# Kernel tuning notes

Hardware: AMD Instinct MI355X
Metric: run time of the kernel (lower is better)

Reference implementation:

```python
import jax, jax.numpy as jnp
import numpy as np

EPS_BN = 1e-5


def _batchnorm(h, g, b):
    # training-mode BatchNorm1d over the flattened (B*N*k) axis
    mu = jnp.mean(h, axis=0)
    var = jnp.var(h, axis=0)
    return g * (h - mu) * jax.lax.rsqrt(var + EPS_BN) + b


def setup_inputs() -> dict:
    key = jax.random.key(0)
    ks = jax.random.split(key, 5)
    B, N = 4, 8192
    x = jax.random.normal(ks[0], (B, N, 3), dtype=jnp.float32)
    W1 = jax.random.normal(ks[1], (7, 10), dtype=jnp.float32) * (1.0 / np.sqrt(7.0))
    b1 = jax.random.normal(ks[2], (10,), dtype=jnp.float32) * 0.01
    W2 = jax.random.normal(ks[3], (10, 10), dtype=jnp.float32) * (1.0 / np.sqrt(10.0))
    b2 = jax.random.normal(ks[4], (10,), dtype=jnp.float32) * 0.01
    g1 = jnp.ones((10,), jnp.float32); be1 = jnp.zeros((10,), jnp.float32)
    g2 = jnp.ones((10,), jnp.float32); be2 = jnp.zeros((10,), jnp.float32)
    return {"x": x, "W1": W1, "b1": b1, "g1": g1, "be1": be1,
            "W2": W2, "b2": b2, "g2": g2, "be2": be2, "k": 9}


def reference(x, W1, b1, g1, be1, W2, b2, g2, be2, k):
    B, N, C = x.shape
    # --- kNN graph (brute force, self included as nearest) ---
    sq = jnp.sum(x * x, axis=-1)                                    # (B,N)
    d2 = sq[:, :, None] + sq[:, None, :] - 2.0 * jnp.einsum('bnc,bmc->bnm', x, x)
    _, idx = jax.lax.top_k(-d2, k + 1)                              # (B,N,k+1)
    nbrs = x[jnp.arange(B)[:, None, None], idx]                     # (B,N,k+1,3)
    rel = (nbrs - x[:, :, None, :])[:, :, 1:, :]                    # drop self -> (B,N,k,3)
    # --- sort neighbors by azimuth phi = atan2(y, x) ---
    phi = jnp.arctan2(rel[..., 1], rel[..., 0])                     # (B,N,k)
    order = jnp.argsort(phi, axis=-1)
    v1 = jnp.take_along_axis(rel, order[..., None], axis=2)         # (B,N,k,3)
    v2 = jnp.roll(v1, -1, axis=2)                                   # next neighbor (cyclic)
    # --- umbrella-style surface features ---
    centroids = 0.5 * (v1 + v2)
    normals = jnp.cross(v1, v2)
    normals = normals / (jnp.linalg.norm(normals, axis=-1, keepdims=True) + 1e-6)
    sign = jnp.where(normals[..., 0:1, 0] > 0, 1.0, -1.0)[..., None]  # (B,N,1,1)
    normals = normals * sign
    position = jnp.sum(normals * centroids, axis=-1, keepdims=True) / jnp.sqrt(jnp.asarray(3.0, x.dtype))
    feat = jnp.concatenate([centroids, normals, position], axis=-1)   # (B,N,k,7)
    feat = feat.reshape(B * N * k, 7)
    # --- tiny MLP + max-pool over k ---
    h = jax.nn.relu(_batchnorm(feat @ W1 + b1, g1, be1))
    h = jax.nn.relu(_batchnorm(h @ W2 + b2, g2, be2))
    return jnp.max(h.reshape(B, N, k, 10), axis=2)                  # (B,N,10)
```

## Files before the change

### kernel.cpp

```cpp
#include <hip/hip_runtime.h>
#include <math.h>
#include <float.h>
#include <stdint.h>

#define B_ 4
#define N_ 8192
#define K_ 9
#define NPTS (B_ * N_)
#define NROWS (NPTS * K_)
#define SPLIT 8
#define CHUNK (N_ / SPLIT)
#define NGROUP 32
#define GSIZE (CHUNK / NGROUP)
#define GSTRIDE 33

__device__ __forceinline__ float dist2f(float4 q, float4 c) {
  float dot = q.x * c.x + q.y * c.y + q.z * c.z;
  return (q.w + c.w) - 2.0f * dot;
}

#define GDECL(G) float gd##G; int gi##G;
#define SCANG(G)                                                           \
  { float bgd = FLT_MAX; int bgi = 0;                                      \
    _Pragma("clang loop unroll(disable)")                                  \
    for (int jj = 0; jj < GSIZE; jj += 4) {                                \
      const float4* cp = CH + (G * GSTRIDE + jj);                          \
      float4 c0 = cp[0], c1 = cp[1], c2 = cp[2], c3 = cp[3];               \
      int j = G * GSIZE + jj;                                              \
      float d0 = dist2f(q, c0), d1 = dist2f(q, c1);                        \
      float d2 = dist2f(q, c2), d3 = dist2f(q, c3);                        \
      if (HS) {                                                            \
        d0 = (j + 0 == nl) ? FLT_MAX : d0;                                 \
        d1 = (j + 1 == nl) ? FLT_MAX : d1;                                 \
        d2 = (j + 2 == nl) ? FLT_MAX : d2;                                 \
        d3 = (j + 3 == nl) ? FLT_MAX : d3;                                 \
      }                                                                    \
      bool l0 = d0 < bgd; bgd = l0 ? d0 : bgd; bgi = l0 ? (j + 0) : bgi;   \
      bool l1 = d1 < bgd; bgd = l1 ? d1 : bgd; bgi = l1 ? (j + 1) : bgi;   \
      bool l2 = d2 < bgd; bgd = l2 ? d2 : bgd; bgi = l2 ? (j + 2) : bgi;   \
      bool l3 = d3 < bgd; bgd = l3 ? d3 : bgd; bgi = l3 ? (j + 3) : bgi;   \
    }                                                                      \
    gd##G = bgd; gi##G = bgi; }
#define LM(G)                                                              \
  { bool lt = gd##G < wd;                                                  \
    wd = lt ? gd##G : wd; wi = lt ? gi##G : wi; wg = lt ? G : wg; }
#define WBK(G)                                                             \
  { bool m = (wg == G); gd##G = m ? nd : gd##G; gi##G = m ? ni : gi##G; }

template <bool HS>
__device__ __forceinline__ void knn_chunk(const float4* CH, float4 q, int nl,
                                          int j0, int s, int p,
                                          uint2* __restrict__ PBDI) {
  GDECL(0) GDECL(1) GDECL(2) GDECL(3) GDECL(4) GDECL(5) GDECL(6) GDECL(7)
  GDECL(8) GDECL(9) GDECL(10) GDECL(11) GDECL(12) GDECL(13) GDECL(14) GDECL(15)
  GDECL(16) GDECL(17) GDECL(18) GDECL(19) GDECL(20) GDECL(21) GDECL(22) GDECL(23)
  GDECL(24) GDECL(25) GDECL(26) GDECL(27) GDECL(28) GDECL(29) GDECL(30) GDECL(31)

  SCANG(0) SCANG(1) SCANG(2) SCANG(3) SCANG(4) SCANG(5) SCANG(6) SCANG(7)
  SCANG(8) SCANG(9) SCANG(10) SCANG(11) SCANG(12) SCANG(13) SCANG(14) SCANG(15)
  SCANG(16) SCANG(17) SCANG(18) SCANG(19) SCANG(20) SCANG(21) SCANG(22) SCANG(23)
  SCANG(24) SCANG(25) SCANG(26) SCANG(27) SCANG(28) SCANG(29) SCANG(30) SCANG(31)

#pragma clang loop unroll(disable)
  for (int r = 0; r < K_; ++r) {
    float wd = gd0; int wi = gi0; int wg = 0;
    LM(1) LM(2) LM(3) LM(4) LM(5) LM(6) LM(7)
    LM(8) LM(9) LM(10) LM(11) LM(12) LM(13) LM(14) LM(15)
    LM(16) LM(17) LM(18) LM(19) LM(20) LM(21) LM(22) LM(23)
    LM(24) LM(25) LM(26) LM(27) LM(28) LM(29) LM(30) LM(31)
    uint2 o; o.x = __float_as_uint(wd); o.y = (unsigned)(j0 + wi);
    PBDI[(size_t)(s * K_ + r) * NPTS + p] = o;

    int ab = wg * GSTRIDE;
    int jb = wg * GSIZE;
    float nd = FLT_MAX; int ni = 0;
#pragma clang loop unroll(disable)
    for (int jj = 0; jj < GSIZE; jj += 4) {
      const float4* cp = CH + (ab + jj);
      float4 c0 = cp[0], c1 = cp[1], c2 = cp[2], c3 = cp[3];
      int j = jb + jj;
      float d0 = dist2f(q, c0), d1 = dist2f(q, c1);
      float d2 = dist2f(q, c2), d3 = dist2f(q, c3);
      if (HS) {
        d0 = (j + 0 == nl) ? FLT_MAX : d0;
        d1 = (j + 1 == nl) ? FLT_MAX : d1;
        d2 = (j + 2 == nl) ? FLT_MAX : d2;
        d3 = (j + 3 == nl) ? FLT_MAX : d3;
      }
      bool k0 = (d0 > wd) | ((d0 == wd) & ((j + 0) > wi));
      bool k1 = (d1 > wd) | ((d1 == wd) & ((j + 1) > wi));
      bool k2 = (d2 > wd) | ((d2 == wd) & ((j + 2) > wi));
      bool k3 = (d3 > wd) | ((d3 == wd) & ((j + 3) > wi));
      d0 = k0 ? d0 : FLT_MAX;
      d1 = k1 ? d1 : FLT_MAX;
      d2 = k2 ? d2 : FLT_MAX;
      d3 = k3 ? d3 : FLT_MAX;
      bool l0 = d0 < nd; nd = l0 ? d0 : nd; ni = l0 ? (j + 0) : ni;
      bool l1 = d1 < nd; nd = l1 ? d1 : nd; ni = l1 ? (j + 1) : ni;
      bool l2 = d2 < nd; nd = l2 ? d2 : nd; ni = l2 ? (j + 2) : ni;
      bool l3 = d3 < nd; nd = l3 ? d3 : nd; ni = l3 ? (j + 3) : ni;
    }
    WBK(0) WBK(1) WBK(2) WBK(3) WBK(4) WBK(5) WBK(6) WBK(7)
    WBK(8) WBK(9) WBK(10) WBK(11) WBK(12) WBK(13) WBK(14) WBK(15)
    WBK(16) WBK(17) WBK(18) WBK(19) WBK(20) WBK(21) WBK(22) WBK(23)
    WBK(24) WBK(25) WBK(26) WBK(27) WBK(28) WBK(29) WBK(30) WBK(31)
  }
}

__launch_bounds__(128, 4)
__global__ void k_knn(const float* __restrict__ x, uint2* __restrict__ PBDI) {
  __shared__ float4 CH[NGROUP * GSTRIDE];
  int bid = blockIdx.x;
  int pg = bid >> 3;
  int s = bid & (SPLIT - 1);
  int p = pg * 128 + threadIdx.x;
  int b = p >> 13;
  int n = p & (N_ - 1);
  int bO = b * N_;
  int j0 = s * CHUNK;

  const float* xq = x + 3 * (size_t)p;
  float qa = xq[0], qb = xq[1], qc = xq[2];
  float4 q = make_float4(qa, qb, qc, qa * qa + qb * qb + qc * qc);

  for (int t = threadIdx.x; t < CHUNK; t += 128) {
    const float* xp = x + 3 * (size_t)(bO + j0 + t);
    float a = xp[0], bb = xp[1], cc = xp[2];
    CH[(t >> 5) * GSTRIDE + (t & 31)] = make_float4(a, bb, cc, a * a + bb * bb + cc * cc);
  }
  __syncthreads();

  int n0 = (pg * 128) & (N_ - 1);
  int nl = n - j0;
  if (s == (n0 >> 10)) knn_chunk<true >(CH, q, nl, j0, s, p, PBDI);
  else                 knn_chunk<false>(CH, q, nl, j0, s, p, PBDI);
}

#define LVL(bdv, biv)                                                     \
  { bool lt = cd < (bdv); float td = (bdv); int ti = (biv);               \
    (bdv) = lt ? cd : (bdv); (biv) = lt ? ci : (biv);                     \
    cd = lt ? td : cd; ci = lt ? ti : ci; }
#define INS9ALL()                                                         \
  LVL(b0d, b0i) LVL(b1d, b1i) LVL(b2d, b2i) LVL(b3d, b3i) LVL(b4d, b4i)  \
  LVL(b5d, b5i) LVL(b6d, b6i) LVL(b7d, b7i) LVL(b8d, b8i)
#define TOP9_DECL()                                                       \
  float b0d = FLT_MAX, b1d = FLT_MAX, b2d = FLT_MAX, b3d = FLT_MAX,       \
        b4d = FLT_MAX, b5d = FLT_MAX, b6d = FLT_MAX, b7d = FLT_MAX,       \
        b8d = FLT_MAX;                                                    \
  int b0i = 0, b1i = 0, b2i = 0, b3i = 0, b4i = 0, b5i = 0, b6i = 0,      \
      b7i = 0, b8i = 0;

#define MKREL(T)                                                          \
  float rx##T, ry##T, rz##T, ph##T;                                       \
  { const float* mp = x + 3 * (size_t)(bO + b##T##i);                     \
    rx##T = mp[0] - qa; ry##T = mp[1] - qb; rz##T = mp[2] - qc;           \
    ph##T = atan2f(ry##T, rx##T); }

#define CE(A, Bv)                                                         \
  { bool lt = ph##Bv < ph##A; float t0;                                   \
    t0 = ph##A; ph##A = lt ? ph##Bv : t0; ph##Bv = lt ? t0 : ph##Bv;      \
    t0 = rx##A; rx##A = lt ? rx##Bv : t0; rx##Bv = lt ? t0 : rx##Bv;      \
    t0 = ry##A; ry##A = lt ? ry##Bv : t0; ry##Bv = lt ? t0 : ry##Bv;      \
    t0 = rz##A; rz##A = lt ? rz##Bv : t0; rz##Bv = lt ? t0 : rz##Bv; }

#define ST9(arr, v0, v1, v2, v3, v4, v5, v6, v7, v8)                      \
  arr[0 * 64 + pl] = v0; arr[1 * 64 + pl] = v1; arr[2 * 64 + pl] = v2;    \
  arr[3 * 64 + pl] = v3; arr[4 * 64 + pl] = v4; arr[5 * 64 + pl] = v5;    \
  arr[6 * 64 + pl] = v6; arr[7 * 64 + pl] = v7; arr[8 * 64 + pl] = v8;

__launch_bounds__(256, 4)
__global__ void k_tail1(const float* __restrict__ x, const uint2* __restrict__ PBDI,
                        const float* __restrict__ W1, const float* __restrict__ b1,
                        float* __restrict__ H1, double* __restrict__ ACC1) {
  __shared__ float  LMD[64 * 37];
  __shared__ int    LMI[64 * 37];
  __shared__ float  LREL[3][9 * 64];
  __shared__ float  LSGN[64];
  __shared__ double sred[4][20];

  int q = threadIdx.x >> 6;
  int pl = threadIdx.x & 63;
  int pbase = blockIdx.x * 64;
  int p = pbase + pl;

  {
    TOP9_DECL();
#pragma clang loop unroll_count(2)
    for (int e = 0; e < 2 * K_; ++e) {
      uint2 v = PBDI[(size_t)(q * 2 * K_ + e) * NPTS + p];
      float cd = __uint_as_float(v.x);
      int ci = (int)v.y;
      INS9ALL();
    }
    int base = pl * 37 + q * 9;
    LMD[base + 0] = b0d; LMD[base + 1] = b1d; LMD[base + 2] = b2d;
    LMD[base + 3] = b3d; LMD[base + 4] = b4d; LMD[base + 5] = b5d;
    LMD[base + 6] = b6d; LMD[base + 7] = b7d; LMD[base + 8] = b8d;
    LMI[base + 0] = b0i; LMI[base + 1] = b1i; LMI[base + 2] = b2i;
    LMI[base + 3] = b3i; LMI[base + 4] = b4i; LMI[base + 5] = b5i;
    LMI[base + 6] = b6i; LMI[base + 7] = b7i; LMI[base + 8] = b8i;
  }
  __syncthreads();

  if (q == 0) {
    int b = p >> 13;
    int bO = b * N_;
    const float* xq = x + 3 * (size_t)p;
    float qa = xq[0], qb = xq[1], qc = xq[2];

    TOP9_DECL();
#pragma clang loop unroll_count(3)
    for (int e = 0; e < 4 * K_; ++e) {
      float cd = LMD[pl * 37 + e];
      int ci = LMI[pl * 37 + e];
      INS9ALL();
    }

    MKREL(0) MKREL(1) MKREL(2) MKREL(3) MKREL(4)
    MKREL(5) MKREL(6) MKREL(7) MKREL(8)

    CE(0,1)
    CE(1,2) CE(0,1)
    CE(2,3) CE(1,2) CE(0,1)
    CE(3,4) CE(2,3) CE(1,2) CE(0,1)
    CE(4,5) CE(3,4) CE(2,3) CE(1,2) CE(0,1)
    CE(5,6) CE(4,5) CE(3,4) CE(2,3) CE(1,2) CE(0,1)
    CE(6,7) CE(5,6) CE(4,5) CE(3,4) CE(2,3) CE(1,2) CE(0,1)
    CE(7,8) CE(6,7) CE(5,6) CE(4,5) CE(3,4) CE(2,3) CE(1,2) CE(0,1)

    float nx0 = ry0 * rz1 - rz0 * ry1;
    float ny0 = rz0 * rx1 - rx0 * rz1;
    float nz0 = rx0 * ry1 - ry0 * rx1;
    float nrm0 = sqrtf(nx0 * nx0 + ny0 * ny0 + nz0 * nz0) + 1e-6f;
    LSGN[pl] = ((nx0 / nrm0) > 0.0f) ? 1.0f : -1.0f;

    ST9(LREL[0], rx0, rx1, rx2, rx3, rx4, rx5, rx6, rx7, rx8)
    ST9(LREL[1], ry0, ry1, ry2, ry3, ry4, ry5, ry6, ry7, ry8)
    ST9(LREL[2], rz0, rz1, rz2, rz3, rz4, rz5, rz6, rz7, rz8)
  }
  __syncthreads();

  double sum[10], ss[10];
#pragma unroll
  for (int c = 0; c < 10; ++c) { sum[c] = 0.0; ss[c] = 0.0; }

#pragma clang loop unroll(disable)
  for (int rl = threadIdx.x; rl < 9 * 64; rl += 256) {
    int t = rl >> 6;
    int pp = rl & 63;
    int t2 = (t + 1 == K_) ? 0 : t + 1;
    float v1x = LREL[0][t * 64 + pp];
    float v1y = LREL[1][t * 64 + pp];
    float v1z = LREL[2][t * 64 + pp];
    float v2x = LREL[0][t2 * 64 + pp];
    float v2y = LREL[1][t2 * 64 + pp];
    float v2z = LREL[2][t2 * 64 + pp];
    float sgn = LSGN[pp];

    float cx = 0.5f * (v1x + v2x);
    float cy = 0.5f * (v1y + v2y);
    float cz = 0.5f * (v1z + v2z);
    float nx = v1y * v2z - v1z * v2y;
    float ny = v1z * v2x - v1x * v2z;
    float nz = v1x * v2y - v1y * v2x;
    float nrm = sqrtf(nx * nx + ny * ny + nz * nz) + 1e-6f;
    nx /= nrm; ny /= nrm; nz /= nrm;
    nx *= sgn; ny *= sgn; nz *= sgn;
    float pos = (nx * cx + ny * cy + nz * cz) / 1.7320508075688772f;

    float fv[7] = {cx, cy, cz, nx, ny, nz, pos};
#pragma unroll
    for (int c = 0; c < 10; ++c) {
      float h = b1[c];
#pragma unroll
      for (int rr = 0; rr < 7; ++rr) h = fmaf(fv[rr], W1[rr * 10 + c], h);
      H1[(size_t)c * NROWS + (size_t)t * NPTS + pbase + pp] = h;
      double hd = (double)h;
      sum[c] += hd; ss[c] += hd * hd;
    }
  }

  int lane = threadIdx.x & 63, wv = threadIdx.x >> 6;
#pragma unroll
  for (int c = 0; c < 10; ++c) {
    double a = sum[c];
#pragma unroll
    for (int off = 32; off > 0; off >>= 1) a += __shfl_down(a, off);
    if (lane == 0) sred[wv][c] = a;
    double qq = ss[c];
#pragma unroll
    for (int off = 32; off > 0; off >>= 1) qq += __shfl_down(qq, off);
    if (lane == 0) sred[wv][10 + c] = qq;
  }
  __syncthreads();
  if (threadIdx.x < 20) {
    atomicAdd(&ACC1[threadIdx.x],
              sred[0][threadIdx.x] + sred[1][threadIdx.x] +
              sred[2][threadIdx.x] + sred[3][threadIdx.x]);
  }
}

__launch_bounds__(256)
__global__ void k_mlp2(const float* __restrict__ H1, const double* __restrict__ ACC1,
                       const float* __restrict__ g1, const float* __restrict__ be1,
                       const float* __restrict__ W2, const float* __restrict__ b2,
                       float* __restrict__ H2, double* __restrict__ ACC2) {
  __shared__ float MR[20];
  if (threadIdx.x < 10) {
    double mu = ACC1[threadIdx.x] / (double)NROWS;
    double var = ACC1[10 + threadIdx.x] / (double)NROWS - mu * mu;
    MR[threadIdx.x] = (float)mu;
    MR[10 + threadIdx.x] = (float)(1.0 / sqrt(var + 1e-5));
  }
  __syncthreads();

  int r = blockIdx.x * 256 + threadIdx.x;
  float v[10];
#pragma unroll
  for (int c = 0; c < 10; ++c) {
    float h = H1[(size_t)c * NROWS + r];
    float z = g1[c] * (h - MR[c]) * MR[10 + c] + be1[c];
    v[c] = z > 0.0f ? z : 0.0f;
  }
  float o[10];
#pragma unroll
  for (int c = 0; c < 10; ++c) {
    float h = b2[c];
#pragma unroll
    for (int t = 0; t < 10; ++t) h = fmaf(v[t], W2[t * 10 + c], h);
    o[c] = h;
    H2[(size_t)c * NROWS + r] = h;
  }

  __shared__ double sred[4][20];
  int lane = threadIdx.x & 63, wv = threadIdx.x >> 6;
#pragma unroll
  for (int c = 0; c < 10; ++c) {
    double a = (double)o[c];
#pragma unroll
    for (int off = 32; off > 0; off >>= 1) a += __shfl_down(a, off);
    if (lane == 0) sred[wv][c] = a;
    double qq = (double)o[c] * (double)o[c];
#pragma unroll
    for (int off = 32; off > 0; off >>= 1) qq += __shfl_down(qq, off);
    if (lane == 0) sred[wv][10 + c] = qq;
  }
  __syncthreads();
  if (threadIdx.x < 20) {
    atomicAdd(&ACC2[threadIdx.x],
              sred[0][threadIdx.x] + sred[1][threadIdx.x] +
              sred[2][threadIdx.x] + sred[3][threadIdx.x]);
  }
}

__launch_bounds__(256)
__global__ void k_out(const float* __restrict__ H2, const double* __restrict__ ACC2,
                      const float* __restrict__ g2, const float* __restrict__ be2,
                      float* __restrict__ out) {
  __shared__ float MR[20];
  if (threadIdx.x < 10) {
    double mu = ACC2[threadIdx.x] / (double)NROWS;
    double var = ACC2[10 + threadIdx.x] / (double)NROWS - mu * mu;
    MR[threadIdx.x] = (float)mu;
    MR[10 + threadIdx.x] = (float)(1.0 / sqrt(var + 1e-5));
  }
  __syncthreads();

  int p = blockIdx.x * 256 + threadIdx.x;
#pragma unroll
  for (int c = 0; c < 10; ++c) {
    float m = -FLT_MAX;
#pragma unroll
    for (int j = 0; j < K_; ++j) {
      float h = H2[(size_t)c * NROWS + j * NPTS + p];
      float z = g2[c] * (h - MR[c]) * MR[10 + c] + be2[c];
      z = z > 0.0f ? z : 0.0f;
      m = fmaxf(m, z);
    }
    out[(size_t)p * 10 + c] = m;
  }
}

extern "C" void kernel_launch(void* const* d_in, const int* in_sizes, int n_in,
                              void* d_out, int out_size, void* d_ws, size_t ws_size,
                              hipStream_t stream) {
  (void)in_sizes; (void)n_in; (void)out_size; (void)ws_size;
  const float* x  = (const float*)d_in[0];
  const float* W1 = (const float*)d_in[1];
  const float* b1 = (const float*)d_in[2];
  const float* g1 = (const float*)d_in[3];
  const float* be1= (const float*)d_in[4];
  const float* W2 = (const float*)d_in[5];
  const float* b2 = (const float*)d_in[6];
  const float* g2 = (const float*)d_in[7];
  const float* be2= (const float*)d_in[8];
  float* out = (float*)d_out;

  char* base = (char*)d_ws;
  uint2*  PBDI = (uint2*)base;
  float*  H1 = (float*)(base + (size_t)SPLIT * K_ * NPTS * 8);
  double* ACC = (double*)(H1 + (size_t)10 * NROWS);
  double* ACC1 = ACC;
  double* ACC2 = ACC + 20;
  float*  H2 = (float*)PBDI;

  hipMemsetAsync(ACC, 0, 40 * sizeof(double), stream);
  k_knn<<<(NPTS / 128) * SPLIT, 128, 0, stream>>>(x, PBDI);
  k_tail1<<<NPTS / 64, 256, 0, stream>>>(x, PBDI, W1, b1, H1, ACC1);
  k_mlp2<<<NROWS / 256, 256, 0, stream>>>(H1, ACC1, g1, be1, W2, b2, H2, ACC2);
  k_out<<<NPTS / 256, 256, 0, stream>>>(H2, ACC2, g2, be2, out);
}
```

Before: 258.7 us.

## Pack kNN candidates as pairs for packed FMA and spread BN atomics

Stores shared-memory candidate points as pairs laid out {x0,x1,y0,y1},{z0,z1,w0,w1}, so distances for two candidates are computed with packed two-wide float FMA operations instead of scalar math. This aims to cut VALU instruction count in the brute-force kNN scan, which dominates the runtime. Separately, the batch-norm statistic atomics are spread across 16 copies by block index and summed by the consumer kernels, to reduce atomic contention on 20 addresses. The price is extra shuffles or register moves if the compiler does not emit packed ops cleanly, plus a slightly larger memset and reduction.

```diff
diff --git a/kernel.cpp b/kernel.cpp
--- a/kernel.cpp
+++ b/kernel.cpp
@@ -13,22 +13,40 @@
 #define NGROUP 32
 #define GSIZE (CHUNK / NGROUP)
 #define GSTRIDE 33
-
-__device__ __forceinline__ float dist2f(float4 q, float4 c) {
-  float dot = q.x * c.x + q.y * c.y + q.z * c.z;
-  return (q.w + c.w) - 2.0f * dot;
+#define NCOPY 16
+
+typedef float f4 __attribute__((ext_vector_type(4)));
+typedef float f32x2 __attribute__((ext_vector_type(2)));
+
+__device__ __forceinline__ f32x2 dist2_pk(f32x2 xx, f32x2 yy, f32x2 zz, f32x2 ww,
+                                          f32x2 qx, f32x2 qy, f32x2 qz, f32x2 qw) {
+  f32x2 t0 = qx * xx;
+  f32x2 t1 = __builtin_elementwise_fma(qy, yy, t0);
+  f32x2 t2 = __builtin_elementwise_fma(qz, zz, t1);
+  f32x2 s  = qw + ww;
+  f32x2 m2 = {-2.0f, -2.0f};
+  return __builtin_elementwise_fma(t2, m2, s);
 }
 
 #define GDECL(G) float gd##G; int gi##G;
 #define SCANG(G)                                                           \
   { float bgd = FLT_MAX; int bgi = 0;                                      \
     _Pragma("clang loop unroll(disable)")                                  \
-    for (int jj = 0; jj < GSIZE; jj += 4) {                                \
-      const float4* cp = CH + (G * GSTRIDE + jj);                          \
-      float4 c0 = cp[0], c1 = cp[1], c2 = cp[2], c3 = cp[3];               \
-      int j = G * GSIZE + jj;                                              \
-      float d0 = dist2f(q, c0), d1 = dist2f(q, c1);                        \
-      float d2 = dist2f(q, c2), d3 = dist2f(q, c3);                        \
+    for (int pr = 0; pr < 16; pr += 2) {                                   \
+      const f4* cp = CH + (G * GSTRIDE + 2 * pr);                          \
+      f4 A0 = cp[0], B0 = cp[1], A1 = cp[2], B1 = cp[3];                   \
+      int j = G * GSIZE + 2 * pr;                                          \
+      f32x2 dA = dist2_pk(__builtin_shufflevector(A0, A0, 0, 1),           \
+                          __builtin_shufflevector(A0, A0, 2, 3),           \
+                          __builtin_shufflevector(B0, B0, 0, 1),           \
+                          __builtin_shufflevector(B0, B0, 2, 3),           \
+                          qx2, qy2, qz2, qw2);                             \
+      f32x2 dB = dist2_pk(__builtin_shufflevector(A1, A1, 0, 1),           \
+                          __builtin_shufflevector(A1, A1, 2, 3),           \
+                          __builtin_shufflevector(B1, B1, 0, 1),           \
+                          __builtin_shufflevector(B1, B1, 2, 3),           \
+                          qx2, qy2, qz2, qw2);                             \
+      float d0 = dA.x, d1 = dA.y, d2 = dB.x, d3 = dB.y;                    \
       if (HS) {                                                            \
         d0 = (j + 0 == nl) ? FLT_MAX : d0;                                 \
         d1 = (j + 1 == nl) ? FLT_MAX : d1;                                 \
@@ -48,8 +66,9 @@
   { bool m = (wg == G); gd##G = m ? nd : gd##G; gi##G = m ? ni : gi##G; }
 
 template <bool HS>
-__device__ __forceinline__ void knn_chunk(const float4* CH, float4 q, int nl,
-                                          int j0, int s, int p,
+__device__ __forceinline__ void knn_chunk(const f4* CH, f32x2 qx2, f32x2 qy2,
+                                          f32x2 qz2, f32x2 qw2,
+                                          int nl, int j0, int s, int p,
                                           uint2* __restrict__ PBDI) {
   GDECL(0) GDECL(1) GDECL(2) GDECL(3) GDECL(4) GDECL(5) GDECL(6) GDECL(7)
   GDECL(8) GDECL(9) GDECL(10) GDECL(11) GDECL(12) GDECL(13) GDECL(14) GDECL(15)
@@ -75,12 +94,21 @@
     int jb = wg * GSIZE;
     float nd = FLT_MAX; int ni = 0;
 #pragma clang loop unroll(disable)
-    for (int jj = 0; jj < GSIZE; jj += 4) {
-      const float4* cp = CH + (ab + jj);
-      float4 c0 = cp[0], c1 = cp[1], c2 = cp[2], c3 = cp[3];
-      int j = jb + jj;
-      float d0 = dist2f(q, c0), d1 = dist2f(q, c1);
-      float d2 = dist2f(q, c2), d3 = dist2f(q, c3);
+    for (int pr = 0; pr < 16; pr += 2) {
+      const f4* cp = CH + (ab + 2 * pr);
+      f4 A0 = cp[0], B0 = cp[1], A1 = cp[2], B1 = cp[3];
+      int j = jb + 2 * pr;
+      f32x2 dA = dist2_pk(__builtin_shufflevector(A0, A0, 0, 1),
+                          __builtin_shufflevector(A0, A0, 2, 3),
+                          __builtin_shufflevector(B0, B0, 0, 1),
+                          __builtin_shufflevector(B0, B0, 2, 3),
+                          qx2, qy2, qz2, qw2);
+      f32x2 dB = dist2_pk(__builtin_shufflevector(A1, A1, 0, 1),
+                          __builtin_shufflevector(A1, A1, 2, 3),
+                          __builtin_shufflevector(B1, B1, 0, 1),
+                          __builtin_shufflevector(B1, B1, 2, 3),
+                          qx2, qy2, qz2, qw2);
+      float d0 = dA.x, d1 = dA.y, d2 = dB.x, d3 = dB.y;
       if (HS) {
         d0 = (j + 0 == nl) ? FLT_MAX : d0;
         d1 = (j + 1 == nl) ? FLT_MAX : d1;
@@ -109,7 +137,7 @@
 
 __launch_bounds__(128, 4)
 __global__ void k_knn(const float* __restrict__ x, uint2* __restrict__ PBDI) {
-  __shared__ float4 CH[NGROUP * GSTRIDE];
+  __shared__ f4 CH[NGROUP * GSTRIDE];
   int bid = blockIdx.x;
   int pg = bid >> 3;
   int s = bid & (SPLIT - 1);
@@ -121,19 +149,25 @@
 
   const float* xq = x + 3 * (size_t)p;
   float qa = xq[0], qb = xq[1], qc = xq[2];
-  float4 q = make_float4(qa, qb, qc, qa * qa + qb * qb + qc * qc);
-
-  for (int t = threadIdx.x; t < CHUNK; t += 128) {
-    const float* xp = x + 3 * (size_t)(bO + j0 + t);
-    float a = xp[0], bb = xp[1], cc = xp[2];
-    CH[(t >> 5) * GSTRIDE + (t & 31)] = make_float4(a, bb, cc, a * a + bb * bb + cc * cc);
+  float qw = qa * qa + qb * qb + qc * qc;
+  f32x2 qx2 = {qa, qa}, qy2 = {qb, qb}, qz2 = {qc, qc}, qw2 = {qw, qw};
+
+  for (int u = threadIdx.x; u < CHUNK / 2; u += 128) {
+    const float* xp = x + 3 * (size_t)(bO + j0 + 2 * u);
+    float a0 = xp[0], b0 = xp[1], c0 = xp[2];
+    float a1 = xp[3], b1 = xp[4], c1 = xp[5];
+    int G = u >> 4, rr = u & 15;
+    f4 lo = {a0, a1, b0, b1};
+    f4 hi = {c0, c1, a0 * a0 + b0 * b0 + c0 * c0, a1 * a1 + b1 * b1 + c1 * c1};
+    CH[G * GSTRIDE + 2 * rr] = lo;
+    CH[G * GSTRIDE + 2 * rr + 1] = hi;
   }
   __syncthreads();
 
   int n0 = (pg * 128) & (N_ - 1);
   int nl = n - j0;
-  if (s == (n0 >> 10)) knn_chunk<true >(CH, q, nl, j0, s, p, PBDI);
-  else                 knn_chunk<false>(CH, q, nl, j0, s, p, PBDI);
+  if (s == (n0 >> 10)) knn_chunk<true >(CH, qx2, qy2, qz2, qw2, nl, j0, s, p, PBDI);
+  else                 knn_chunk<false>(CH, qx2, qy2, qz2, qw2, nl, j0, s, p, PBDI);
 }
 
 #define LVL(bdv, biv)                                                     \
@@ -171,7 +205,7 @@
 __launch_bounds__(256, 4)
 __global__ void k_tail1(const float* __restrict__ x, const uint2* __restrict__ PBDI,
                         const float* __restrict__ W1, const float* __restrict__ b1,
-                        float* __restrict__ H1, double* __restrict__ ACC1) {
+                        float* __restrict__ H1, double* __restrict__ ACC) {
   __shared__ float  LMD[64 * 37];
   __shared__ int    LMI[64 * 37];
   __shared__ float  LREL[3][9 * 64];
@@ -294,21 +328,27 @@
   }
   __syncthreads();
   if (threadIdx.x < 20) {
-    atomicAdd(&ACC1[threadIdx.x],
+    atomicAdd(&ACC[(blockIdx.x & (NCOPY - 1)) * 40 + threadIdx.x],
               sred[0][threadIdx.x] + sred[1][threadIdx.x] +
               sred[2][threadIdx.x] + sred[3][threadIdx.x]);
   }
 }
 
 __launch_bounds__(256)
-__global__ void k_mlp2(const float* __restrict__ H1, const double* __restrict__ ACC1,
+__global__ void k_mlp2(const float* __restrict__ H1, double* __restrict__ ACC,
                        const float* __restrict__ g1, const float* __restrict__ be1,
                        const float* __restrict__ W2, const float* __restrict__ b2,
-                       float* __restrict__ H2, double* __restrict__ ACC2) {
+                       float* __restrict__ H2) {
   __shared__ float MR[20];
   if (threadIdx.x < 10) {
-    double mu = ACC1[threadIdx.x] / (double)NROWS;
-    double var = ACC1[10 + threadIdx.x] / (double)NROWS - mu * mu;
+    double s0 = 0.0, s1 = 0.0;
+#pragma unroll
+    for (int cc = 0; cc < NCOPY; ++cc) {
+      s0 += ACC[cc * 40 + threadIdx.x];
+      s1 += ACC[cc * 40 + 10 + threadIdx.x];
+    }
+    double mu = s0 / (double)NROWS;
+    double var = s1 / (double)NROWS - mu * mu;
     MR[threadIdx.x] = (float)mu;
     MR[10 + threadIdx.x] = (float)(1.0 / sqrt(var + 1e-5));
   }
@@ -347,20 +387,26 @@
   }
   __syncthreads();
   if (threadIdx.x < 20) {
-    atomicAdd(&ACC2[threadIdx.x],
+    atomicAdd(&ACC[(blockIdx.x & (NCOPY - 1)) * 40 + 20 + threadIdx.x],
               sred[0][threadIdx.x] + sred[1][threadIdx.x] +
               sred[2][threadIdx.x] + sred[3][threadIdx.x]);
   }
 }
 
 __launch_bounds__(256)
-__global__ void k_out(const float* __restrict__ H2, const double* __restrict__ ACC2,
+__global__ void k_out(const float* __restrict__ H2, const double* __restrict__ ACC,
                       const float* __restrict__ g2, const float* __restrict__ be2,
                       float* __restrict__ out) {
   __shared__ float MR[20];
   if (threadIdx.x < 10) {
-    double mu = ACC2[threadIdx.x] / (double)NROWS;
-    double var = ACC2[10 + threadIdx.x] / (double)NROWS - mu * mu;
+    double s0 = 0.0, s1 = 0.0;
+#pragma unroll
+    for (int cc = 0; cc < NCOPY; ++cc) {
+      s0 += ACC[cc * 40 + 20 + threadIdx.x];
+      s1 += ACC[cc * 40 + 30 + threadIdx.x];
+    }
+    double mu = s0 / (double)NROWS;
+    double var = s1 / (double)NROWS - mu * mu;
     MR[threadIdx.x] = (float)mu;
     MR[10 + threadIdx.x] = (float)(1.0 / sqrt(var + 1e-5));
   }
@@ -400,13 +446,11 @@
   uint2*  PBDI = (uint2*)base;
   float*  H1 = (float*)(base + (size_t)SPLIT * K_ * NPTS * 8);
   double* ACC = (double*)(H1 + (size_t)10 * NROWS);
-  double* ACC1 = ACC;
-  double* ACC2 = ACC + 20;
   float*  H2 = (float*)PBDI;
 
-  hipMemsetAsync(ACC, 0, 40 * sizeof(double), stream);
+  hipMemsetAsync(ACC, 0, NCOPY * 40 * sizeof(double), stream);
   k_knn<<<(NPTS / 128) * SPLIT, 128, 0, stream>>>(x, PBDI);
-  k_tail1<<<NPTS / 64, 256, 0, stream>>>(x, PBDI, W1, b1, H1, ACC1);
-  k_mlp2<<<NROWS / 256, 256, 0, stream>>>(H1, ACC1, g1, be1, W2, b2, H2, ACC2);
-  k_out<<<NPTS / 256, 256, 0, stream>>>(H2, ACC2, g2, be2, out);
-}
+  k_tail1<<<NPTS / 64, 256, 0, stream>>>(x, PBDI, W1, b1, H1, ACC);
+  k_mlp2<<<NROWS / 256, 256, 0, stream>>>(H1, ACC, g1, be1, W2, b2, H2);
+  k_out<<<NPTS / 256, 256, 0, stream>>>(H2, ACC, g2, be2, out);
+}
```

Result: faster. 237.6 us (-8.1%).
